# Kernel optimization log

Measured on AMD Instinct MI355X. Metric: run time of the kernel, lower is better.

The kernel has to match this reference:

```python
import jax, jax.numpy as jnp
import numpy as np

N_USERS = 50000
N_ENT = 200000
N = N_USERS + N_ENT
D = 128
E = 2_000_000
B = 8192
NCAT = 8
CATV = 1000
NNUM = 16
H = 2 * D  # n_hiddens = 2 * embed_dim


def setup_inputs() -> dict:
    key = jax.random.key(0)
    ks = jax.random.split(key, 32)
    s = 0.02
    inp = {}
    inp['entity_user_embed'] = jax.random.normal(ks[0], (N, D), jnp.float32) * s
    inp['A_vals'] = jax.random.uniform(ks[1], (E,), jnp.float32) / 8.0
    # category embedding tables; row 0 is padding -> zeros
    inp['user_cat_table'] = (jax.random.normal(ks[2], (CATV + 1, D), jnp.float32) * s).at[0].set(0.0)
    inp['item_cat_table'] = (jax.random.normal(ks[3], (CATV + 1, D), jnp.float32) * s).at[0].set(0.0)
    inp['num_W_user'] = jax.random.normal(ks[4], (D, NNUM), jnp.float32) * s
    inp['num_b_user'] = jax.random.normal(ks[5], (D,), jnp.float32) * s
    inp['num_W_item'] = jax.random.normal(ks[6], (D, NNUM), jnp.float32) * s
    inp['num_b_item'] = jax.random.normal(ks[7], (D,), jnp.float32) * s
    # MaskLinear stack: (2D->H), (H->H), (H->1); masks stacked over 2 tasks
    inp['W0'] = jax.random.normal(ks[8], (H, 2 * D), jnp.float32) * s
    inp['b0'] = jax.random.normal(ks[9], (H,), jnp.float32) * s
    inp['Mw0'] = jax.random.normal(ks[10], (2, H, 2 * D), jnp.float32)
    inp['Mb0'] = jax.random.normal(ks[11], (2, H), jnp.float32)
    inp['W1'] = jax.random.normal(ks[12], (H, H), jnp.float32) * s
    inp['b1'] = jax.random.normal(ks[13], (H,), jnp.float32) * s
    inp['Mw1'] = jax.random.normal(ks[14], (2, H, H), jnp.float32)
    inp['Mb1'] = jax.random.normal(ks[15], (2, H), jnp.float32)
    inp['W2'] = jax.random.normal(ks[16], (1, H), jnp.float32) * s
    inp['b2'] = jax.random.normal(ks[17], (1,), jnp.float32) * s
    inp['Mw2'] = jax.random.normal(ks[18], (2, 1, H), jnp.float32)
    inp['Mb2'] = jax.random.normal(ks[19], (2, 1), jnp.float32)
    inp['user_num_feats'] = jax.random.normal(ks[20], (N_USERS, NNUM), jnp.float32)
    inp['item_num_feats'] = jax.random.normal(ks[21], (N_ENT, NNUM), jnp.float32)
    inp['A_rows'] = jax.random.randint(ks[22], (E,), 0, N, jnp.int32)
    inp['A_cols'] = jax.random.randint(ks[23], (E,), 0, N, jnp.int32)
    # category ids; 0 means padding (some zeros occur naturally)
    inp['user_cat_feats'] = jax.random.randint(ks[24], (N_USERS, NCAT), 0, CATV + 1, jnp.int32)
    inp['item_cat_feats'] = jax.random.randint(ks[25], (N_ENT, NCAT), 0, CATV + 1, jnp.int32)
    inp['user_ids'] = jax.random.randint(ks[26], (B,), 0, N_USERS, jnp.int32)  # offset by N_ENT inside
    inp['item_ids'] = jax.random.randint(ks[27], (B,), 0, N_ENT, jnp.int32)
    return inp


def _mask_linear(x, W, b, Mw, Mb, task):
    # F.linear(x, W * sigmoid(mask_w[task]), b * sigmoid(mask_b[task]))
    return x @ (W * jax.nn.sigmoid(Mw[task])).T + b * jax.nn.sigmoid(Mb[task])


def _category_features(cat_ids, table):
    # padded-embedding mean over nonzero ids (get_category_features)
    emb = table[cat_ids]                               # [B, F, D] (row 0 is zeros)
    cnt = jnp.sum(cat_ids > 0, axis=-1).astype(jnp.float32)
    inv = jnp.where(cnt > 0, 1.0 / jnp.maximum(cnt, 1.0), 0.0)  # nan_to_num(1/cnt)
    return jnp.sum(emb, axis=1) * inv[:, None]          # [B, D]


def _side(all_embed, ids, cat_ids, num_feats, cat_table, num_W, num_b,
          W0, b0, Mw0, Mb0, W1, b1, Mw1, Mb1, W2, b2, Mw2, Mb2, task):
    embed = all_embed[ids]                              # [B, D]
    feat = _category_features(cat_ids, cat_table)
    feat = feat + jax.nn.relu(num_feats @ num_W.T + num_b)
    x = jnp.concatenate([embed, feat], axis=-1)         # [B, 2D]
    h = jax.nn.relu(_mask_linear(x, W0, b0, Mw0, Mb0, task))
    h = jax.nn.relu(_mask_linear(h, W1, b1, Mw1, Mb1, task))
    w = jax.nn.sigmoid(_mask_linear(h, W2, b2, Mw2, Mb2, task))  # [B, 1]
    return w * embed + (1.0 - w) * feat


def reference(entity_user_embed, A_vals, user_cat_table, item_cat_table,
              num_W_user, num_b_user, num_W_item, num_b_item,
              W0, b0, Mw0, Mb0, W1, b1, Mw1, Mb1, W2, b2, Mw2, Mb2,
              user_num_feats, item_num_feats,
              A_rows, A_cols, user_cat_feats, item_cat_feats, user_ids, item_ids):
    # sparse KGAT-style propagation: agg = A_in @ ego
    msgs = A_vals[:, None] * entity_user_embed[A_cols]           # [E, D]
    agg = jax.ops.segment_sum(msgs, A_rows, num_segments=N)       # [N, D]
    all_embed = entity_user_embed + agg

    u_ids_global = user_ids + N_ENT  # user ids live after entities in the table
    u = _side(all_embed, u_ids_global, user_cat_feats[user_ids], user_num_feats[user_ids],
              user_cat_table, num_W_user, num_b_user,
              W0, b0, Mw0, Mb0, W1, b1, Mw1, Mb1, W2, b2, Mw2, Mb2, task=0)
    i = _side(all_embed, item_ids, item_cat_feats[item_ids], item_num_feats[item_ids],
              item_cat_table, num_W_item, num_b_item,
              W0, b0, Mw0, Mb0, W1, b1, Mw1, Mb1, W2, b2, Mw2, Mb2, task=1)
    return jnp.sum(u * i, axis=-1)  # [B] CF scores
```

## Files before the change

kernel.cpp:

```cpp
#include <hip/hip_runtime.h>
#include <math.h>

#define N_USERS 50000
#define N_ENT   200000
#define NTOT    250000
#define D       128
#define E_EDGES 2000000
#define B       8192
#define NCAT    8
#define NNUM    16
#define CAP     64
#define BR      32

typedef __attribute__((ext_vector_type(4))) float f32x4;
typedef __attribute__((ext_vector_type(8))) short short8;

__device__ __forceinline__ float sigf(float x) { return 1.0f / (1.0f + expf(-x)); }

__device__ __forceinline__ short f2bf(float f) {
    unsigned u = __float_as_uint(f);
    unsigned r = (u + 0x7FFF + ((u >> 16) & 1)) >> 16;
    return (short)r;
}
__device__ __forceinline__ unsigned pack_bf2(float lo, float hi) {
    return ((unsigned)(unsigned short)f2bf(hi) << 16) | (unsigned short)f2bf(lo);
}
__device__ __forceinline__ float bf_lo(unsigned x) { return __uint_as_float(x << 16); }
__device__ __forceinline__ float bf_hi(unsigned x) { return __uint_as_float(x & 0xFFFF0000u); }
__device__ __forceinline__ float dot4(float4 a, float4 b) {
    return a.x * b.x + a.y * b.y + a.z * b.z + a.w * b.w;
}

__global__ __launch_bounds__(256) void init_weff_kernel(
    int* __restrict__ map, int* __restrict__ bincnt,
    const float* __restrict__ W0, const float* __restrict__ Mw0,
    const float* __restrict__ b0, const float* __restrict__ Mb0,
    const float* __restrict__ W1, const float* __restrict__ Mw1,
    const float* __restrict__ b1, const float* __restrict__ Mb1,
    const float* __restrict__ W2, const float* __restrict__ Mw2,
    const float* __restrict__ b2, const float* __restrict__ Mb2,
    short* __restrict__ W0h, short* __restrict__ W1h, float* __restrict__ w2eff,
    float* __restrict__ beff0, float* __restrict__ beff1, float* __restrict__ b2eff)
{
    int t = blockIdx.x * 256 + threadIdx.x;
    if (t < 62500) {
        ((int4*)map)[t] = make_int4(-1, -1, -1, -1);
        return;
    }
    t -= 62500;
    if (t < 4096) {
        ((int4*)bincnt)[t] = make_int4(0, 0, 0, 0);
        return;
    }
    int i = t - 4096;
    if (i < 131072) {
        W0h[i] = f2bf(W0[i & 65535] * sigf(Mw0[i]));
    } else if (i < 262144) {
        int ii = i - 131072;
        W1h[ii] = f2bf(W1[ii & 65535] * sigf(Mw1[ii]));
    } else if (i < 262656) {
        int ii = i - 262144;
        w2eff[ii] = W2[ii & 255] * sigf(Mw2[ii]);
    } else if (i < 263168) {
        int ii = i - 262656;
        beff0[ii] = b0[ii & 255] * sigf(Mb0[ii]);
    } else if (i < 263680) {
        int ii = i - 263168;
        beff1[ii] = b1[ii & 255] * sigf(Mb1[ii]);
    } else if (i < 263682) {
        int ii = i - 263680;
        b2eff[ii] = b2[0] * sigf(Mb2[ii]);
    }
}

__global__ __launch_bounds__(256) void build_map_kernel(
    const int* __restrict__ uids, const int* __restrict__ iids, int* __restrict__ map)
{
    int b = blockIdx.x * 256 + threadIdx.x;
    if (b < B) {
        atomicMax(&map[uids[b] + N_ENT], b);
        atomicMax(&map[iids[b]], B + b);
    }
}

__global__ __launch_bounds__(256) void scatter_kernel(
    const int* __restrict__ A_rows, const int* __restrict__ A_cols,
    const float* __restrict__ A_vals, const int* __restrict__ map,
    int* __restrict__ bincnt, int2* __restrict__ bins)
{
    const int g = blockIdx.x * 256 + threadIdx.x;
    if (g >= E_EDGES / 2) return;
    const int2 rr = *(const int2*)(A_rows + 2 * g);
    const int s0 = map[rr.x];
    const int s1 = map[rr.y];
    if (s0 >= 0) {
        const int p = atomicAdd(&bincnt[s0], 1);
        if (p < CAP)
            bins[(size_t)s0 * CAP + p] = make_int2(A_cols[2 * g], __float_as_int(A_vals[2 * g]));
    }
    if (s1 >= 0) {
        const int p = atomicAdd(&bincnt[s1], 1);
        if (p < CAP)
            bins[(size_t)s1 * CAP + p] = make_int2(A_cols[2 * g + 1], __float_as_int(A_vals[2 * g + 1]));
    }
}

__global__ __launch_bounds__(256) void build_x_kernel(
    const int* __restrict__ uids, const int* __restrict__ iids,
    const int* __restrict__ u_catf, const int* __restrict__ i_catf,
    const float* __restrict__ u_numf, const float* __restrict__ i_numf,
    const float* __restrict__ u_tab, const float* __restrict__ i_tab,
    const float* __restrict__ numW_u, const float* __restrict__ numb_u,
    const float* __restrict__ numW_i, const float* __restrict__ numb_i,
    const float* __restrict__ embed, const int* __restrict__ map,
    const int* __restrict__ bincnt, const int2* __restrict__ bins,
    unsigned short* __restrict__ Xu, unsigned short* __restrict__ Xi)
{
    const int wid  = (blockIdx.x * 256 + threadIdx.x) >> 6;
    const int lane = threadIdx.x & 63;
    const int side = wid & 1;
    const int b    = wid >> 1;
    const int d2   = lane * 2;

    const int* ids = side ? iids : uids;
    const int* cat_feats = side ? i_catf : u_catf;
    const float* num_feats = side ? i_numf : u_numf;
    const float* cat_table = side ? i_tab : u_tab;
    const float* numW = side ? numW_i : numW_u;
    const float* numb = side ? numb_i : numb_u;
    unsigned short* Xo = side ? Xi : Xu;

    const int uid  = __builtin_amdgcn_readfirstlane(ids[b]);
    const int grow = uid + (side ? 0 : N_ENT);
    const int slot = __builtin_amdgcn_readfirstlane(map[grow]);
    const int n    = min(__builtin_amdgcn_readfirstlane(bincnt[slot]), CAP);

    const float2 ev0 = *(const float2*)(embed + (size_t)grow * D + d2);
    const int4* bl4 = (const int4*)(bins + (size_t)slot * CAP);
    const int4 ea = bl4[0], eb = bl4[1], ec = bl4[2], ed = bl4[3];
    const int4 cf0 = *(const int4*)(cat_feats + uid * NCAT);
    const int4 cf1 = *(const int4*)(cat_feats + uid * NCAT + 4);
    const float4* nf = (const float4*)(num_feats + (size_t)uid * NNUM);
    const float4 f0 = nf[0], f1 = nf[1], f2v = nf[2], f3 = nf[3];
    const float2 nbv = *(const float2*)(numb + d2);

    float gx = 0.f, gy = 0.f;
    {
        int  cc[8]; float vv[8];
        cc[0]=ea.x; vv[0]=__int_as_float(ea.y); cc[1]=ea.z; vv[1]=__int_as_float(ea.w);
        cc[2]=eb.x; vv[2]=__int_as_float(eb.y); cc[3]=eb.z; vv[3]=__int_as_float(eb.w);
        cc[4]=ec.x; vv[4]=__int_as_float(ec.y); cc[5]=ec.z; vv[5]=__int_as_float(ec.w);
        cc[6]=ed.x; vv[6]=__int_as_float(ed.y); cc[7]=ed.z; vv[7]=__int_as_float(ed.w);
        float2 r[8];
#pragma unroll
        for (int j = 0; j < 8; ++j) {
            const int c = (j < n) ? cc[j] : 0;
            r[j] = *(const float2*)(embed + (size_t)c * D + d2);
        }
#pragma unroll
        for (int j = 0; j < 8; ++j) {
            const float v = (j < n) ? vv[j] : 0.f;
            gx += v * r[j].x;
            gy += v * r[j].y;
        }
    }
    const int2* bl = bins + (size_t)slot * CAP;
    for (int j = 8; j < n; j += 2) {
        const int2 c0 = bl[j];
        const bool has1 = (j + 1 < n);
        const int2 c1 = has1 ? bl[j + 1] : make_int2(0, 0);
        const float2 r0 = *(const float2*)(embed + (size_t)c0.x * D + d2);
        const float2 r1 = *(const float2*)(embed + (size_t)c1.x * D + d2);
        const float v0 = __int_as_float(c0.y);
        const float v1 = has1 ? __int_as_float(c1.y) : 0.f;
        gx += v0 * r0.x + v1 * r1.x;
        gy += v0 * r0.y + v1 * r1.y;
    }

    int cid[8] = {cf0.x, cf0.y, cf0.z, cf0.w, cf1.x, cf1.y, cf1.z, cf1.w};
    int cnt = 0;
#pragma unroll
    for (int f = 0; f < 8; ++f) cnt += (cid[f] > 0);
    float2 ct[8];
#pragma unroll
    for (int f = 0; f < 8; ++f)
        ct[f] = *(const float2*)(cat_table + (size_t)cid[f] * D + d2);
    float csx = 0.f, csy = 0.f;
#pragma unroll
    for (int f = 0; f < 8; ++f) { csx += ct[f].x; csy += ct[f].y; }
    const float inv = (cnt > 0) ? (1.0f / (float)cnt) : 0.0f;

    const float4* w0r = (const float4*)(numW + (size_t)d2 * NNUM);
    const float4* w1r = (const float4*)(numW + (size_t)(d2 + 1) * NNUM);
    float na = nbv.x + dot4(w0r[0], f0) + dot4(w0r[1], f1) + dot4(w0r[2], f2v) + dot4(w0r[3], f3);
    float nb_ = nbv.y + dot4(w1r[0], f0) + dot4(w1r[1], f1) + dot4(w1r[2], f2v) + dot4(w1r[3], f3);

    const float fx = csx * inv + fmaxf(na, 0.f);
    const float fy = csy * inv + fmaxf(nb_, 0.f);

    unsigned short* row = Xo + (size_t)b * 256;
    *(unsigned*)(row + d2)       = pack_bf2(ev0.x + gx, ev0.y + gy);
    *(unsigned*)(row + 128 + d2) = pack_bf2(fx, fy);
}

__global__ __launch_bounds__(256) void fused_mlp_kernel(
    const unsigned short* __restrict__ Xu, const unsigned short* __restrict__ Xi,
    const short* __restrict__ W0h, const short* __restrict__ W1h,
    const float* __restrict__ beff0, const float* __restrict__ beff1,
    const float* __restrict__ w2eff, const float* __restrict__ b2eff,
    float* __restrict__ w_u, float* __restrict__ w_i)
{
    const int side = blockIdx.y;
    const unsigned short* Xg = side ? Xi : Xu;
    float* wout = side ? w_i : w_u;
    const int b0 = blockIdx.x * BR;

    __shared__ __align__(16) short Xs[BR * 256];
    __shared__ float gsum[4][BR];

    const int tid = threadIdx.x;
    const int w   = tid >> 6;
    const int l   = tid & 63;
    const int l15 = l & 15;
    const int l4  = l >> 4;

#pragma unroll
    for (int i = 0; i < 4; ++i) {
        const int ch  = tid + i * 256;
        const int row = ch >> 5;
        const int c8  = (ch & 31) << 3;
        const short8 hv = *(const short8*)(Xg + (size_t)(b0 + row) * 256 + c8);
        const int byte = row * 512 + ((c8 * 2) ^ ((row & 7) << 4));
        *(short8*)((char*)Xs + byte) = hv;
    }
    __syncthreads();

    const short* W0l = W0h + (size_t)side * 65536;
    const short* W1l = W1h + (size_t)side * 65536;
    const int cwbase = w * 64;

    f32x4 acc[2][4];
#pragma unroll
    for (int m = 0; m < 2; ++m)
#pragma unroll
        for (int n = 0; n < 4; ++n) acc[m][n] = (f32x4){0.f, 0.f, 0.f, 0.f};

#pragma unroll
    for (int ks = 0; ks < 8; ++ks) {
        short8 a[2];
#pragma unroll
        for (int m = 0; m < 2; ++m) {
            const int row = m * 16 + l15;
            const int kb  = ks * 64 + l4 * 16;
            a[m] = *(const short8*)((const char*)Xs + row * 512 + (kb ^ ((row & 7) << 4)));
        }
#pragma unroll
        for (int n = 0; n < 4; ++n) {
            const short8 bb = *(const short8*)(W0l + (size_t)(cwbase + n * 16 + l15) * 256 + ks * 32 + l4 * 8);
            acc[0][n] = __builtin_amdgcn_mfma_f32_16x16x32_bf16(a[0], bb, acc[0][n], 0, 0, 0);
            acc[1][n] = __builtin_amdgcn_mfma_f32_16x16x32_bf16(a[1], bb, acc[1][n], 0, 0, 0);
        }
    }
    __syncthreads();

#pragma unroll
    for (int n = 0; n < 4; ++n) {
        const int col = cwbase + n * 16 + l15;
        const float bia = beff0[side * 256 + col];
#pragma unroll
        for (int m = 0; m < 2; ++m)
#pragma unroll
            for (int r = 0; r < 4; ++r) {
                const float v = fmaxf(acc[m][n][r] + bia, 0.f);
                const int row = m * 16 + l4 * 4 + r;
                const int byte = row * 512 + ((col * 2) ^ ((row & 7) << 4));
                *(short*)((char*)Xs + byte) = f2bf(v);
            }
    }
    __syncthreads();

#pragma unroll
    for (int m = 0; m < 2; ++m)
#pragma unroll
        for (int n = 0; n < 4; ++n) acc[m][n] = (f32x4){0.f, 0.f, 0.f, 0.f};

#pragma unroll
    for (int ks = 0; ks < 8; ++ks) {
        short8 a[2];
#pragma unroll
        for (int m = 0; m < 2; ++m) {
            const int row = m * 16 + l15;
            const int kb  = ks * 64 + l4 * 16;
            a[m] = *(const short8*)((const char*)Xs + row * 512 + (kb ^ ((row & 7) << 4)));
        }
#pragma unroll
        for (int n = 0; n < 4; ++n) {
            const short8 bb = *(const short8*)(W1l + (size_t)(cwbase + n * 16 + l15) * 256 + ks * 32 + l4 * 8);
            acc[0][n] = __builtin_amdgcn_mfma_f32_16x16x32_bf16(a[0], bb, acc[0][n], 0, 0, 0);
            acc[1][n] = __builtin_amdgcn_mfma_f32_16x16x32_bf16(a[1], bb, acc[1][n], 0, 0, 0);
        }
    }

    float w2v[4], b1v[4];
#pragma unroll
    for (int n = 0; n < 4; ++n) {
        const int col = cwbase + n * 16 + l15;
        w2v[n] = w2eff[side * 256 + col];
        b1v[n] = beff1[side * 256 + col];
    }
#pragma unroll
    for (int m = 0; m < 2; ++m)
#pragma unroll
        for (int r = 0; r < 4; ++r) {
            float s = fmaxf(acc[m][0][r] + b1v[0], 0.f) * w2v[0]
                    + fmaxf(acc[m][1][r] + b1v[1], 0.f) * w2v[1]
                    + fmaxf(acc[m][2][r] + b1v[2], 0.f) * w2v[2]
                    + fmaxf(acc[m][3][r] + b1v[3], 0.f) * w2v[3];
            s += __shfl_xor(s, 1, 16);
            s += __shfl_xor(s, 2, 16);
            s += __shfl_xor(s, 4, 16);
            s += __shfl_xor(s, 8, 16);
            if (l15 == 0) gsum[w][m * 16 + l4 * 4 + r] = s;
        }
    __syncthreads();
    if (tid < BR) {
        const float s = gsum[0][tid] + gsum[1][tid] + gsum[2][tid] + gsum[3][tid]
                      + b2eff[side];
        wout[b0 + tid] = 1.0f / (1.0f + expf(-s));
    }
}

__global__ __launch_bounds__(256) void dot_kernel(
    const unsigned short* __restrict__ Xu, const unsigned short* __restrict__ Xi,
    const float* __restrict__ wu, const float* __restrict__ wi,
    float* __restrict__ out)
{
    const int tid = threadIdx.x;
    const int wv = tid >> 6, lane = tid & 63;
    const int b = blockIdx.x * 4 + wv;
    const float a = wu[b], c = wi[b];
    const unsigned short* xu = Xu + (size_t)b * 256;
    const unsigned short* xi = Xi + (size_t)b * 256;
    const unsigned ue = *(const unsigned*)(xu + 2 * lane);
    const unsigned uf = *(const unsigned*)(xu + 128 + 2 * lane);
    const unsigned ie = *(const unsigned*)(xi + 2 * lane);
    const unsigned jf = *(const unsigned*)(xi + 128 + 2 * lane);
    const float u0 = a * bf_lo(ue) + (1.f - a) * bf_lo(uf);
    const float u1 = a * bf_hi(ue) + (1.f - a) * bf_hi(uf);
    const float v0 = c * bf_lo(ie) + (1.f - c) * bf_lo(jf);
    const float v1 = c * bf_hi(ie) + (1.f - c) * bf_hi(jf);
    float s = u0 * v0 + u1 * v1;
#pragma unroll
    for (int off = 32; off > 0; off >>= 1) s += __shfl_xor(s, off, 64);
    if (lane == 0) out[b] = s;
}

extern "C" void kernel_launch(void* const* d_in, const int* in_sizes, int n_in,
                              void* d_out, int out_size, void* d_ws, size_t ws_size,
                              hipStream_t stream)
{
    const float* embed    = (const float*)d_in[0];
    const float* A_vals   = (const float*)d_in[1];
    const float* u_cat_tab= (const float*)d_in[2];
    const float* i_cat_tab= (const float*)d_in[3];
    const float* numW_u   = (const float*)d_in[4];
    const float* numb_u   = (const float*)d_in[5];
    const float* numW_i   = (const float*)d_in[6];
    const float* numb_i   = (const float*)d_in[7];
    const float* W0  = (const float*)d_in[8];
    const float* b0  = (const float*)d_in[9];
    const float* Mw0 = (const float*)d_in[10];
    const float* Mb0 = (const float*)d_in[11];
    const float* W1  = (const float*)d_in[12];
    const float* b1  = (const float*)d_in[13];
    const float* Mw1 = (const float*)d_in[14];
    const float* Mb1 = (const float*)d_in[15];
    const float* W2  = (const float*)d_in[16];
    const float* b2  = (const float*)d_in[17];
    const float* Mw2 = (const float*)d_in[18];
    const float* Mb2 = (const float*)d_in[19];
    const float* u_numf = (const float*)d_in[20];
    const float* i_numf = (const float*)d_in[21];
    const int* A_rows = (const int*)d_in[22];
    const int* A_cols = (const int*)d_in[23];
    const int* u_catf = (const int*)d_in[24];
    const int* i_catf = (const int*)d_in[25];
    const int* u_ids  = (const int*)d_in[26];
    const int* i_ids  = (const int*)d_in[27];
    float* out = (float*)d_out;

    char* ws = (char*)d_ws;
    size_t off = 0;
    auto alloc = [&](size_t bytes) -> void* {
        void* p = ws + off;
        off += (bytes + 255) & ~(size_t)255;
        return p;
    };
    int*   map     = (int*)  alloc((size_t)NTOT * 4);
    int*   bincnt  = (int*)  alloc((size_t)2 * B * 4);
    int2*  bins    = (int2*) alloc((size_t)2 * B * CAP * 8);
    short* W0h     = (short*)alloc((size_t)2 * 65536 * 2);
    short* W1h     = (short*)alloc((size_t)2 * 65536 * 2);
    float* w2eff   = (float*)alloc(512 * 4);
    float* beff0   = (float*)alloc(512 * 4);
    float* beff1   = (float*)alloc(512 * 4);
    float* b2eff   = (float*)alloc(2 * 4);
    unsigned short* Xu = (unsigned short*)alloc((size_t)B * 256 * 2);
    unsigned short* Xi = (unsigned short*)alloc((size_t)B * 256 * 2);
    float* w_u     = (float*)alloc((size_t)B * 4);
    float* w_i     = (float*)alloc((size_t)B * 4);

    init_weff_kernel<<<1291, 256, 0, stream>>>(
        map, bincnt,
        W0, Mw0, b0, Mb0, W1, Mw1, b1, Mb1, W2, Mw2, b2, Mb2,
        W0h, W1h, w2eff, beff0, beff1, b2eff);

    build_map_kernel<<<(B + 255) / 256, 256, 0, stream>>>(u_ids, i_ids, map);

    scatter_kernel<<<(E_EDGES / 2 + 255) / 256, 256, 0, stream>>>(
        A_rows, A_cols, A_vals, map, bincnt, bins);

    build_x_kernel<<<(2 * B) / 4, 256, 0, stream>>>(
        u_ids, i_ids, u_catf, i_catf, u_numf, i_numf, u_cat_tab, i_cat_tab,
        numW_u, numb_u, numW_i, numb_i, embed, map, bincnt, bins, Xu, Xi);

    dim3 mgrid(B / BR, 2);
    fused_mlp_kernel<<<mgrid, 256, 0, stream>>>(
        Xu, Xi, W0h, W1h, beff0, beff1, w2eff, b2eff, w_u, w_i);

    dot_kernel<<<B / 4, 256, 0, stream>>>(Xu, Xi, w_u, w_i, out);
}
```

Baseline: 83.63 us.

## Fuse MLP gate and final dot product into one kernel per row tile

Merges the per-side MLP kernel and the dot kernel into a single kernel. Each block loads both user and item X tiles into shared memory, runs the two-layer MLP for both sides in sequence, keeps the gate weights in shared memory, and computes the final scores from the X tiles already staged there. This removes one kernel launch, the w_u/w_i round trip through global memory, and the second read of Xu/Xi. In exchange the grid is halved (256 blocks instead of 512), the two sides run serially inside each block, and shared memory per block grows to about 48KB, which may cut occupancy.

```diff
diff --git a/kernel.cpp b/kernel.cpp
--- a/kernel.cpp
+++ b/kernel.cpp
@@ -146,7 +146,7 @@
 
     float gx = 0.f, gy = 0.f;
     {
-        int  cc[8]; float vv[8];
+        int cc[8]; float vv[8];
         cc[0]=ea.x; vv[0]=__int_as_float(ea.y); cc[1]=ea.z; vv[1]=__int_as_float(ea.w);
         cc[2]=eb.x; vv[2]=__int_as_float(eb.y); cc[3]=eb.z; vv[3]=__int_as_float(eb.w);
         cc[4]=ec.x; vv[4]=__int_as_float(ec.y); cc[5]=ec.z; vv[5]=__int_as_float(ec.w);
@@ -192,7 +192,7 @@
 
     const float4* w0r = (const float4*)(numW + (size_t)d2 * NNUM);
     const float4* w1r = (const float4*)(numW + (size_t)(d2 + 1) * NNUM);
-    float na = nbv.x + dot4(w0r[0], f0) + dot4(w0r[1], f1) + dot4(w0r[2], f2v) + dot4(w0r[3], f3);
+    float na  = nbv.x + dot4(w0r[0], f0) + dot4(w0r[1], f1) + dot4(w0r[2], f2v) + dot4(w0r[3], f3);
     float nb_ = nbv.y + dot4(w1r[0], f0) + dot4(w1r[1], f1) + dot4(w1r[2], f2v) + dot4(w1r[3], f3);
 
     const float fx = csx * inv + fmaxf(na, 0.f);
@@ -203,20 +203,19 @@
     *(unsigned*)(row + 128 + d2) = pack_bf2(fx, fy);
 }
 
-__global__ __launch_bounds__(256) void fused_mlp_kernel(
+__global__ __launch_bounds__(256) void fused_mlp_dot_kernel(
     const unsigned short* __restrict__ Xu, const unsigned short* __restrict__ Xi,
     const short* __restrict__ W0h, const short* __restrict__ W1h,
     const float* __restrict__ beff0, const float* __restrict__ beff1,
     const float* __restrict__ w2eff, const float* __restrict__ b2eff,
-    float* __restrict__ w_u, float* __restrict__ w_i)
-{
-    const int side = blockIdx.y;
-    const unsigned short* Xg = side ? Xi : Xu;
-    float* wout = side ? w_i : w_u;
-    const int b0 = blockIdx.x * BR;
-
-    __shared__ __align__(16) short Xs[BR * 256];
+    float* __restrict__ out)
+{
+    const int r0 = blockIdx.x * BR;
+
+    __shared__ __align__(16) short XsE[2 * BR * 256];
+    __shared__ __align__(16) short Hs[BR * 256];
     __shared__ float gsum[4][BR];
+    __shared__ float w_s[2][BR];
 
     const int tid = threadIdx.x;
     const int w   = tid >> 6;
@@ -225,134 +224,132 @@
     const int l4  = l >> 4;
 
 #pragma unroll
-    for (int i = 0; i < 4; ++i) {
-        const int ch  = tid + i * 256;
-        const int row = ch >> 5;
-        const int c8  = (ch & 31) << 3;
-        const short8 hv = *(const short8*)(Xg + (size_t)(b0 + row) * 256 + c8);
-        const int byte = row * 512 + ((c8 * 2) ^ ((row & 7) << 4));
-        *(short8*)((char*)Xs + byte) = hv;
+    for (int i = 0; i < 8; ++i) {
+        const int ch   = tid + i * 256;
+        const int side = ch >> 10;
+        const int c    = ch & 1023;
+        const int row  = c >> 5;
+        const int c8   = (c & 31) << 3;
+        const unsigned short* Xg = side ? Xi : Xu;
+        const short8 hv = *(const short8*)(Xg + (size_t)(r0 + row) * 256 + c8);
+        const int byte = side * 16384 + row * 512 + ((c8 * 2) ^ ((row & 7) << 4));
+        *(short8*)((char*)XsE + byte) = hv;
     }
     __syncthreads();
 
-    const short* W0l = W0h + (size_t)side * 65536;
-    const short* W1l = W1h + (size_t)side * 65536;
     const int cwbase = w * 64;
-
-    f32x4 acc[2][4];
-#pragma unroll
-    for (int m = 0; m < 2; ++m)
-#pragma unroll
-        for (int n = 0; n < 4; ++n) acc[m][n] = (f32x4){0.f, 0.f, 0.f, 0.f};
-
-#pragma unroll
-    for (int ks = 0; ks < 8; ++ks) {
-        short8 a[2];
-#pragma unroll
-        for (int m = 0; m < 2; ++m) {
-            const int row = m * 16 + l15;
-            const int kb  = ks * 64 + l4 * 16;
-            a[m] = *(const short8*)((const char*)Xs + row * 512 + (kb ^ ((row & 7) << 4)));
-        }
+    for (int side = 0; side < 2; ++side) {
+        const short* W0l = W0h + side * 65536;
+        const short* W1l = W1h + side * 65536;
+
+        f32x4 acc[2][4];
+#pragma unroll
+        for (int m = 0; m < 2; ++m)
+#pragma unroll
+            for (int n = 0; n < 4; ++n) acc[m][n] = (f32x4){0.f, 0.f, 0.f, 0.f};
+
+#pragma unroll
+        for (int ks = 0; ks < 8; ++ks) {
+            short8 a[2];
+#pragma unroll
+            for (int m = 0; m < 2; ++m) {
+                const int row = m * 16 + l15;
+                const int kb  = ks * 64 + l4 * 16;
+                a[m] = *(const short8*)((const char*)XsE + side * 16384 + row * 512 + (kb ^ ((row & 7) << 4)));
+            }
+#pragma unroll
+            for (int n = 0; n < 4; ++n) {
+                const short8 bb = *(const short8*)(W0l + (size_t)(cwbase + n * 16 + l15) * 256 + ks * 32 + l4 * 8);
+                acc[0][n] = __builtin_amdgcn_mfma_f32_16x16x32_bf16(a[0], bb, acc[0][n], 0, 0, 0);
+                acc[1][n] = __builtin_amdgcn_mfma_f32_16x16x32_bf16(a[1], bb, acc[1][n], 0, 0, 0);
+            }
+        }
+        __syncthreads();
+
 #pragma unroll
         for (int n = 0; n < 4; ++n) {
-            const short8 bb = *(const short8*)(W0l + (size_t)(cwbase + n * 16 + l15) * 256 + ks * 32 + l4 * 8);
-            acc[0][n] = __builtin_amdgcn_mfma_f32_16x16x32_bf16(a[0], bb, acc[0][n], 0, 0, 0);
-            acc[1][n] = __builtin_amdgcn_mfma_f32_16x16x32_bf16(a[1], bb, acc[1][n], 0, 0, 0);
-        }
-    }
-    __syncthreads();
-
-#pragma unroll
-    for (int n = 0; n < 4; ++n) {
-        const int col = cwbase + n * 16 + l15;
-        const float bia = beff0[side * 256 + col];
+            const int col = cwbase + n * 16 + l15;
+            const float bia = beff0[side * 256 + col];
+#pragma unroll
+            for (int m = 0; m < 2; ++m)
+#pragma unroll
+                for (int r = 0; r < 4; ++r) {
+                    const float v = fmaxf(acc[m][n][r] + bia, 0.f);
+                    const int row = m * 16 + l4 * 4 + r;
+                    const int byte = row * 512 + ((col * 2) ^ ((row & 7) << 4));
+                    *(short*)((char*)Hs + byte) = f2bf(v);
+                }
+        }
+        __syncthreads();
+
 #pragma unroll
         for (int m = 0; m < 2; ++m)
 #pragma unroll
+            for (int n = 0; n < 4; ++n) acc[m][n] = (f32x4){0.f, 0.f, 0.f, 0.f};
+#pragma unroll
+        for (int ks = 0; ks < 8; ++ks) {
+            short8 a[2];
+#pragma unroll
+            for (int m = 0; m < 2; ++m) {
+                const int row = m * 16 + l15;
+                const int kb  = ks * 64 + l4 * 16;
+                a[m] = *(const short8*)((const char*)Hs + row * 512 + (kb ^ ((row & 7) << 4)));
+            }
+#pragma unroll
+            for (int n = 0; n < 4; ++n) {
+                const short8 bb = *(const short8*)(W1l + (size_t)(cwbase + n * 16 + l15) * 256 + ks * 32 + l4 * 8);
+                acc[0][n] = __builtin_amdgcn_mfma_f32_16x16x32_bf16(a[0], bb, acc[0][n], 0, 0, 0);
+                acc[1][n] = __builtin_amdgcn_mfma_f32_16x16x32_bf16(a[1], bb, acc[1][n], 0, 0, 0);
+            }
+        }
+
+        float w2v[4], b1v[4];
+#pragma unroll
+        for (int n = 0; n < 4; ++n) {
+            const int col = cwbase + n * 16 + l15;
+            w2v[n] = w2eff[side * 256 + col];
+            b1v[n] = beff1[side * 256 + col];
+        }
+#pragma unroll
+        for (int m = 0; m < 2; ++m)
+#pragma unroll
             for (int r = 0; r < 4; ++r) {
-                const float v = fmaxf(acc[m][n][r] + bia, 0.f);
-                const int row = m * 16 + l4 * 4 + r;
-                const int byte = row * 512 + ((col * 2) ^ ((row & 7) << 4));
-                *(short*)((char*)Xs + byte) = f2bf(v);
+                float s = fmaxf(acc[m][0][r] + b1v[0], 0.f) * w2v[0]
+                        + fmaxf(acc[m][1][r] + b1v[1], 0.f) * w2v[1]
+                        + fmaxf(acc[m][2][r] + b1v[2], 0.f) * w2v[2]
+                        + fmaxf(acc[m][3][r] + b1v[3], 0.f) * w2v[3];
+                s += __shfl_xor(s, 1, 16);
+                s += __shfl_xor(s, 2, 16);
+                s += __shfl_xor(s, 4, 16);
+                s += __shfl_xor(s, 8, 16);
+                if (l15 == 0) gsum[w][m * 16 + l4 * 4 + r] = s;
             }
-    }
-    __syncthreads();
-
-#pragma unroll
-    for (int m = 0; m < 2; ++m)
-#pragma unroll
-        for (int n = 0; n < 4; ++n) acc[m][n] = (f32x4){0.f, 0.f, 0.f, 0.f};
-
-#pragma unroll
-    for (int ks = 0; ks < 8; ++ks) {
-        short8 a[2];
-#pragma unroll
-        for (int m = 0; m < 2; ++m) {
-            const int row = m * 16 + l15;
-            const int kb  = ks * 64 + l4 * 16;
-            a[m] = *(const short8*)((const char*)Xs + row * 512 + (kb ^ ((row & 7) << 4)));
-        }
-#pragma unroll
-        for (int n = 0; n < 4; ++n) {
-            const short8 bb = *(const short8*)(W1l + (size_t)(cwbase + n * 16 + l15) * 256 + ks * 32 + l4 * 8);
-            acc[0][n] = __builtin_amdgcn_mfma_f32_16x16x32_bf16(a[0], bb, acc[0][n], 0, 0, 0);
-            acc[1][n] = __builtin_amdgcn_mfma_f32_16x16x32_bf16(a[1], bb, acc[1][n], 0, 0, 0);
-        }
-    }
-
-    float w2v[4], b1v[4];
-#pragma unroll
-    for (int n = 0; n < 4; ++n) {
-        const int col = cwbase + n * 16 + l15;
-        w2v[n] = w2eff[side * 256 + col];
-        b1v[n] = beff1[side * 256 + col];
-    }
-#pragma unroll
-    for (int m = 0; m < 2; ++m)
-#pragma unroll
-        for (int r = 0; r < 4; ++r) {
-            float s = fmaxf(acc[m][0][r] + b1v[0], 0.f) * w2v[0]
-                    + fmaxf(acc[m][1][r] + b1v[1], 0.f) * w2v[1]
-                    + fmaxf(acc[m][2][r] + b1v[2], 0.f) * w2v[2]
-                    + fmaxf(acc[m][3][r] + b1v[3], 0.f) * w2v[3];
-            s += __shfl_xor(s, 1, 16);
-            s += __shfl_xor(s, 2, 16);
-            s += __shfl_xor(s, 4, 16);
-            s += __shfl_xor(s, 8, 16);
-            if (l15 == 0) gsum[w][m * 16 + l4 * 4 + r] = s;
-        }
-    __syncthreads();
-    if (tid < BR) {
-        const float s = gsum[0][tid] + gsum[1][tid] + gsum[2][tid] + gsum[3][tid]
-                      + b2eff[side];
-        wout[b0 + tid] = 1.0f / (1.0f + expf(-s));
-    }
-}
-
-__global__ __launch_bounds__(256) void dot_kernel(
-    const unsigned short* __restrict__ Xu, const unsigned short* __restrict__ Xi,
-    const float* __restrict__ wu, const float* __restrict__ wi,
-    float* __restrict__ out)
-{
-    const int tid = threadIdx.x;
-    const int wv = tid >> 6, lane = tid & 63;
-    const int b = blockIdx.x * 4 + wv;
-    const float a = wu[b], c = wi[b];
-    const unsigned short* xu = Xu + (size_t)b * 256;
-    const unsigned short* xi = Xi + (size_t)b * 256;
-    const unsigned ue = *(const unsigned*)(xu + 2 * lane);
-    const unsigned uf = *(const unsigned*)(xu + 128 + 2 * lane);
-    const unsigned ie = *(const unsigned*)(xi + 2 * lane);
-    const unsigned jf = *(const unsigned*)(xi + 128 + 2 * lane);
-    const float u0 = a * bf_lo(ue) + (1.f - a) * bf_lo(uf);
-    const float u1 = a * bf_hi(ue) + (1.f - a) * bf_hi(uf);
-    const float v0 = c * bf_lo(ie) + (1.f - c) * bf_lo(jf);
-    const float v1 = c * bf_hi(ie) + (1.f - c) * bf_hi(jf);
-    float s = u0 * v0 + u1 * v1;
-#pragma unroll
-    for (int off = 32; off > 0; off >>= 1) s += __shfl_xor(s, off, 64);
-    if (lane == 0) out[b] = s;
+        __syncthreads();
+        if (tid < BR)
+            w_s[side][tid] = 1.0f / (1.0f + expf(-(gsum[0][tid] + gsum[1][tid]
+                             + gsum[2][tid] + gsum[3][tid] + b2eff[side])));
+        __syncthreads();
+    }
+
+    const int d2 = l * 2;
+#pragma unroll
+    for (int q = 0; q < 8; ++q) {
+        const int row = w * 8 + q;
+        const int sw = (row & 7) << 4;
+        const unsigned ue = *(const unsigned*)((const char*)XsE + row * 512 + ((d2 * 2) ^ sw));
+        const unsigned uf = *(const unsigned*)((const char*)XsE + row * 512 + (((128 + d2) * 2) ^ sw));
+        const unsigned ie = *(const unsigned*)((const char*)XsE + 16384 + row * 512 + ((d2 * 2) ^ sw));
+        const unsigned jf = *(const unsigned*)((const char*)XsE + 16384 + row * 512 + (((128 + d2) * 2) ^ sw));
+        const float a = w_s[0][row], c = w_s[1][row];
+        const float u0 = a * bf_lo(ue) + (1.f - a) * bf_lo(uf);
+        const float u1 = a * bf_hi(ue) + (1.f - a) * bf_hi(uf);
+        const float v0 = c * bf_lo(ie) + (1.f - c) * bf_lo(jf);
+        const float v1 = c * bf_hi(ie) + (1.f - c) * bf_hi(jf);
+        float s = u0 * v0 + u1 * v1;
+#pragma unroll
+        for (int off = 32; off > 0; off >>= 1) s += __shfl_xor(s, off, 64);
+        if (l == 0) out[r0 + row] = s;
+    }
 }
 
 extern "C" void kernel_launch(void* const* d_in, const int* in_sizes, int n_in,
@@ -407,8 +404,6 @@
     float* b2eff   = (float*)alloc(2 * 4);
     unsigned short* Xu = (unsigned short*)alloc((size_t)B * 256 * 2);
     unsigned short* Xi = (unsigned short*)alloc((size_t)B * 256 * 2);
-    float* w_u     = (float*)alloc((size_t)B * 4);
-    float* w_i     = (float*)alloc((size_t)B * 4);
 
     init_weff_kernel<<<1291, 256, 0, stream>>>(
         map, bincnt,
@@ -424,9 +419,6 @@
         u_ids, i_ids, u_catf, i_catf, u_numf, i_numf, u_cat_tab, i_cat_tab,
         numW_u, numb_u, numW_i, numb_i, embed, map, bincnt, bins, Xu, Xi);
 
-    dim3 mgrid(B / BR, 2);
-    fused_mlp_kernel<<<mgrid, 256, 0, stream>>>(
-        Xu, Xi, W0h, W1h, beff0, beff1, w2eff, b2eff, w_u, w_i);
-
-    dot_kernel<<<B / 4, 256, 0, stream>>>(Xu, Xi, w_u, w_i, out);
-}
+    fused_mlp_dot_kernel<<<B / BR, 256, 0, stream>>>(
+        Xu, Xi, W0h, W1h, beff0, beff1, w2eff, b2eff, out);
+}
```

Result: slower. 99.32 us (+18.8%).
